# Performance work log

Measured on AMD Instinct MI355X. Metric: run time of the kernel, lower is better.

## Reference

```python
import jax, jax.numpy as jnp
import numpy as np
import math

B, T, IN_DIM, HID = 32, 1024, 512, 512
TAU_MEM = 20.0
THRESHOLD = 1.0
ALPHA = math.exp(-1.0 / TAU_MEM)


def setup_inputs() -> dict:
    key = jax.random.key(0)
    kx, kw, kb = jax.random.split(key, 3)
    bound = 1.0 / math.sqrt(IN_DIM)
    x = jax.random.normal(kx, (B, T, IN_DIM), dtype=jnp.float32)
    W = jax.random.uniform(kw, (HID, IN_DIM), minval=-bound, maxval=bound, dtype=jnp.float32)
    b = jax.random.uniform(kb, (HID,), minval=-bound, maxval=bound, dtype=jnp.float32)
    threshold_adapt = jnp.ones((HID,), dtype=jnp.float32) * THRESHOLD
    return {"x": x, "W": W, "b": b, "threshold_adapt": threshold_adapt}


def reference(x, W, b, threshold_adapt):
    # Precompute the batched GEMM for all timesteps: z[b,t,h]
    z = jnp.einsum('bti,hi->bth', x, W) + b
    thr = threshold_adapt[None, :]  # [1,H]

    def step(mem, z_t):
        # leaky integrate
        mem = ALPHA * mem + z_t              # [B,H]
        spike = (mem >= thr).astype(mem.dtype)
        mem = mem * (1.0 - spike)            # hard reset
        return mem, spike

    mem0 = jnp.zeros((x.shape[0], W.shape[0]), dtype=x.dtype)
    # scan over time axis: z transposed to [T,B,H]
    mem_final, spikes = jax.lax.scan(step, mem0, jnp.swapaxes(z, 0, 1))
    spikes = jnp.swapaxes(spikes, 0, 1)      # [B,T,H]
    return spikes, mem_final
```

## Files before the change

### kernel.cpp

```cpp
#include <hip/hip_runtime.h>
#include <cstdint>
#include <cstddef>

#define BATCH  32
#define TSTEPS 1024
#define INDIM  512
#define HIDDIM 512
#define MTOT   (BATCH * TSTEPS)

#define MB 128
#define NB 128
#define KC 32
#define KTILES (INDIM / KC)
#define NBLK   (HIDDIM / NB)

constexpr float ALPHA = 0.951229424500714f;

__device__ __forceinline__ int swzg(int g) { return g ^ (g >> 3); }

__global__ __launch_bounds__(256)
void snn_gemm(const float* __restrict__ x, const float* __restrict__ W,
              float* __restrict__ z)
{
    __shared__ float Asm[KC][MB];
    __shared__ float Bsm[KC][NB];

    const int tid = threadIdx.x;
    const int mb  = blockIdx.x / NBLK;
    const int nb  = blockIdx.x % NBLK;
    const int m0  = mb * MB;
    const int n0  = nb * NB;

    const int sr = tid >> 1;
    const int sc = (tid & 1) * 4;
    const int srg = sr >> 2;
    const int swr = (swzg(srg) << 2) | (sr & 3);

    const float4* Ag = reinterpret_cast<const float4*>(x + (size_t)(m0 + sr) * INDIM) + sc;
    const float4* Bg = reinterpret_cast<const float4*>(W + (size_t)(n0 + sr) * INDIM) + sc;

    const int cm = (tid >> 4) * 8;
    const int cn = (tid & 15) * 8;
    const int am0 = swzg(cm >> 2);
    const int am1 = swzg((cm >> 2) + 1);
    const int bn0 = swzg(cn >> 2);
    const int bn1 = swzg((cn >> 2) + 1);

    float acc[8][8];
#pragma unroll
    for (int i = 0; i < 8; ++i)
#pragma unroll
        for (int j = 0; j < 8; ++j) acc[i][j] = 0.0f;

    float4 sa[4], sb[4];
#pragma unroll
    for (int j = 0; j < 4; ++j) { sa[j] = Ag[j]; sb[j] = Bg[j]; }

    for (int kt = 0; kt < KTILES; ++kt) {
        __syncthreads();
#pragma unroll
        for (int j = 0; j < 4; ++j) {
            const int kq = (sc + j) * 4;
            Asm[kq + 0][swr] = sa[j].x;
            Asm[kq + 1][swr] = sa[j].y;
            Asm[kq + 2][swr] = sa[j].z;
            Asm[kq + 3][swr] = sa[j].w;
            Bsm[kq + 0][swr] = sb[j].x;
            Bsm[kq + 1][swr] = sb[j].y;
            Bsm[kq + 2][swr] = sb[j].z;
            Bsm[kq + 3][swr] = sb[j].w;
        }
        __syncthreads();

        if (kt + 1 < KTILES) {
            Ag += KC / 4;
            Bg += KC / 4;
#pragma unroll
            for (int j = 0; j < 4; ++j) { sa[j] = Ag[j]; sb[j] = Bg[j]; }
        }

#pragma unroll 8
        for (int kc = 0; kc < KC; ++kc) {
            const float4* Ar = reinterpret_cast<const float4*>(&Asm[kc][0]);
            const float4* Br = reinterpret_cast<const float4*>(&Bsm[kc][0]);
            float4 a0 = Ar[am0];
            float4 a1 = Ar[am1];
            float4 b0 = Br[bn0];
            float4 b1 = Br[bn1];
            const float av[8] = {a0.x, a0.y, a0.z, a0.w, a1.x, a1.y, a1.z, a1.w};
            const float bv[8] = {b0.x, b0.y, b0.z, b0.w, b1.x, b1.y, b1.z, b1.w};
#pragma unroll
            for (int i = 0; i < 8; ++i)
#pragma unroll
                for (int j = 0; j < 8; ++j)
                    acc[i][j] = fmaf(av[i], bv[j], acc[i][j]);
        }
    }

#pragma unroll
    for (int i = 0; i < 8; ++i) {
        float* zr = z + (size_t)(m0 + cm + i) * HIDDIM + n0 + cn;
        float4 v0 = {acc[i][0], acc[i][1], acc[i][2], acc[i][3]};
        float4 v1 = {acc[i][4], acc[i][5], acc[i][6], acc[i][7]};
        *reinterpret_cast<float4*>(zr)     = v0;
        *reinterpret_cast<float4*>(zr + 4) = v1;
    }
}

#define SCAND 8

__global__ __launch_bounds__(64)
void snn_scan(const float* zsrc, float* out,
              const float* __restrict__ bias, const float* __restrict__ thr)
{
    const int h = (blockIdx.x & 7) * 64 + threadIdx.x;
    const int b = blockIdx.x >> 3;

    const float bb = bias[h];
    const float tt = thr[h];
    float mem = 0.0f;

    const size_t base = ((size_t)b * TSTEPS) * HIDDIM + h;
    const float* zp = zsrc + base;
    float* sp = out + base;

    float pf[SCAND][8];

#pragma unroll
    for (int g = 0; g < SCAND; ++g)
#pragma unroll
        for (int j = 0; j < 8; ++j)
            pf[g][j] = zp[(size_t)(g * 8 + j) * HIDDIM];

#pragma unroll 8
    for (int t8 = 0; t8 < 120; ++t8) {
        const int slot = t8 & (SCAND - 1);
        float cur[8];
#pragma unroll
        for (int j = 0; j < 8; ++j) cur[j] = pf[slot][j];
#pragma unroll
        for (int j = 0; j < 8; ++j)
            pf[slot][j] = zp[(size_t)((t8 + SCAND) * 8 + j) * HIDDIM];
#pragma unroll
        for (int j = 0; j < 8; ++j) {
            float zv = cur[j] + bb;
            mem = fmaf(ALPHA, mem, zv);
            bool s = (mem >= tt);
            sp[(size_t)(t8 * 8 + j) * HIDDIM] = s ? 1.0f : 0.0f;
            mem = s ? 0.0f : mem;
        }
    }

#pragma unroll
    for (int t8 = 120; t8 < 128; ++t8) {
        const int slot = t8 & (SCAND - 1);
#pragma unroll
        for (int j = 0; j < 8; ++j) {
            float zv = pf[slot][j] + bb;
            mem = fmaf(ALPHA, mem, zv);
            bool s = (mem >= tt);
            sp[(size_t)(t8 * 8 + j) * HIDDIM] = s ? 1.0f : 0.0f;
            mem = s ? 0.0f : mem;
        }
    }

    out[(size_t)MTOT * HIDDIM + (size_t)b * HIDDIM + h] = mem;
}

extern "C" void kernel_launch(void* const* d_in, const int* in_sizes, int n_in,
                              void* d_out, int out_size, void* d_ws, size_t ws_size,
                              hipStream_t stream)
{
    const float* x    = (const float*)d_in[0];
    const float* W    = (const float*)d_in[1];
    const float* bias = (const float*)d_in[2];
    const float* thr  = (const float*)d_in[3];
    float* out = (float*)d_out;

    (void)in_sizes; (void)n_in; (void)out_size;

    const size_t z_bytes = (size_t)MTOT * HIDDIM * sizeof(float);
    const bool use_ws = (ws_size >= z_bytes);
    float* zbuf = use_ws ? (float*)d_ws : out;

    dim3 ggrid((MTOT / MB) * NBLK);
    hipLaunchKernelGGL(snn_gemm, ggrid, dim3(256), 0, stream, x, W, zbuf);

    dim3 sgrid(BATCH * (HIDDIM / 64));
    hipLaunchKernelGGL(snn_scan, sgrid, dim3(64), 0, stream, zbuf, out, bias, thr);
}
```

Measured before the change: 326.7 us.

## Warp-specialize scan kernel with producer wave staging z chunks into LDS

The recurrent scan kernel now uses 128-thread blocks. One wave issues vectorized float4 global loads of 32-timestep chunks of z into a double-buffered LDS tile, while the other wave runs the serial leaky-integrate recurrence reading from LDS. This replaces the per-thread scalar register prefetch ring. The goal is to hide global load latency behind the serial dependency chain and use wider loads. In exchange it adds a block barrier every chunk and LDS traffic, and only half the threads do the scan arithmetic.

```diff
diff --git a/kernel.cpp b/kernel.cpp
--- a/kernel.cpp
+++ b/kernel.cpp
@@ -13,6 +13,10 @@
 #define KC 32
 #define KTILES (INDIM / KC)
 #define NBLK   (HIDDIM / NB)
+
+#define SH 64
+#define ST 32
+#define SNC (TSTEPS / ST)
 
 constexpr float ALPHA = 0.951229424500714f;
 
@@ -41,10 +45,8 @@
 
     const int cm = (tid >> 4) * 8;
     const int cn = (tid & 15) * 8;
-    const int am0 = swzg(cm >> 2);
-    const int am1 = swzg((cm >> 2) + 1);
-    const int bn0 = swzg(cn >> 2);
-    const int bn1 = swzg((cn >> 2) + 1);
+    const int am0 = swzg(cm >> 2), am1 = swzg((cm >> 2) + 1);
+    const int bn0 = swzg(cn >> 2), bn1 = swzg((cn >> 2) + 1);
 
     float acc[8][8];
 #pragma unroll
@@ -107,64 +109,91 @@
     }
 }
 
-#define SCAND 8
-
-__global__ __launch_bounds__(64)
-void snn_scan(const float* zsrc, float* out,
+#define LWRITE(BUF, R)                                                        \
+    _Pragma("unroll")                                                         \
+    for (int j = 0; j < 8; ++j)                                               \
+        *reinterpret_cast<float4*>(&zl[BUF][j * 4 + tr][hc]) = R[j];
+
+#define GLOAD(R, C)                                                           \
+    _Pragma("unroll")                                                         \
+    for (int j = 0; j < 8; ++j)                                               \
+        R[j] = *reinterpret_cast<const float4*>(                              \
+            zbase + (size_t)((C) * ST + j * 4 + tr) * HIDDIM + hc);
+
+#define SCAN_CHUNK(BUF, C)                                                    \
+    {                                                                         \
+        float* orow = obase + (size_t)(C) * ST * HIDDIM + lane;               \
+        _Pragma("unroll 8")                                                   \
+        for (int r = 0; r < ST; ++r) {                                        \
+            float zv = zl[BUF][r][lane] + bb;                                 \
+            mem = fmaf(ALPHA, mem, zv);                                       \
+            bool s = (mem >= tt);                                             \
+            orow[(size_t)r * HIDDIM] = s ? 1.0f : 0.0f;                       \
+            mem = s ? 0.0f : mem;                                             \
+        }                                                                     \
+    }
+
+#define FENCE_BARRIER()                                                       \
+    asm volatile("s_waitcnt lgkmcnt(0)" ::: "memory");                        \
+    __builtin_amdgcn_sched_barrier(0);                                        \
+    __builtin_amdgcn_s_barrier();
+
+__global__ __launch_bounds__(128)
+void snn_scan(const float* __restrict__ zsrc, float* __restrict__ out,
               const float* __restrict__ bias, const float* __restrict__ thr)
 {
-    const int h = (blockIdx.x & 7) * 64 + threadIdx.x;
-    const int b = blockIdx.x >> 3;
-
-    const float bb = bias[h];
-    const float tt = thr[h];
+    __shared__ float zl[2][ST][SH];
+
+    const int tid  = threadIdx.x;
+    const int lane = tid & 63;
+    const int wave = tid >> 6;
+    const int b    = blockIdx.x >> 3;
+    const int h0   = (blockIdx.x & 7) * SH;
+
+    const float* zbase = zsrc + (size_t)b * TSTEPS * HIDDIM + h0;
+    float*       obase = out  + (size_t)b * TSTEPS * HIDDIM + h0;
+
+    const int tr = lane >> 4;
+    const int hc = (lane & 15) * 4;
+
+    const float bb = (wave == 0) ? bias[h0 + lane] : 0.0f;
+    const float tt = (wave == 0) ? thr[h0 + lane]  : 1.0e30f;
     float mem = 0.0f;
 
-    const size_t base = ((size_t)b * TSTEPS) * HIDDIM + h;
-    const float* zp = zsrc + base;
-    float* sp = out + base;
-
-    float pf[SCAND][8];
-
-#pragma unroll
-    for (int g = 0; g < SCAND; ++g)
-#pragma unroll
-        for (int j = 0; j < 8; ++j)
-            pf[g][j] = zp[(size_t)(g * 8 + j) * HIDDIM];
-
-#pragma unroll 8
-    for (int t8 = 0; t8 < 120; ++t8) {
-        const int slot = t8 & (SCAND - 1);
-        float cur[8];
-#pragma unroll
-        for (int j = 0; j < 8; ++j) cur[j] = pf[slot][j];
-#pragma unroll
-        for (int j = 0; j < 8; ++j)
-            pf[slot][j] = zp[(size_t)((t8 + SCAND) * 8 + j) * HIDDIM];
-#pragma unroll
-        for (int j = 0; j < 8; ++j) {
-            float zv = cur[j] + bb;
-            mem = fmaf(ALPHA, mem, zv);
-            bool s = (mem >= tt);
-            sp[(size_t)(t8 * 8 + j) * HIDDIM] = s ? 1.0f : 0.0f;
-            mem = s ? 0.0f : mem;
-        }
-    }
-
-#pragma unroll
-    for (int t8 = 120; t8 < 128; ++t8) {
-        const int slot = t8 & (SCAND - 1);
-#pragma unroll
-        for (int j = 0; j < 8; ++j) {
-            float zv = pf[slot][j] + bb;
-            mem = fmaf(ALPHA, mem, zv);
-            bool s = (mem >= tt);
-            sp[(size_t)(t8 * 8 + j) * HIDDIM] = s ? 1.0f : 0.0f;
-            mem = s ? 0.0f : mem;
-        }
-    }
-
-    out[(size_t)MTOT * HIDDIM + (size_t)b * HIDDIM + h] = mem;
+    float4 ra[8], rb[8];
+
+    if (wave == 1) {
+        GLOAD(ra, 0)
+        GLOAD(rb, 1)
+        __builtin_amdgcn_sched_barrier(0);
+        LWRITE(0, ra)
+    }
+    FENCE_BARRIER();
+
+    for (int cc = 0; cc < SNC / 2; ++cc) {
+        const int c = 2 * cc;
+
+        if (wave == 1) {
+            if (c + 2 < SNC) { GLOAD(ra, c + 2) }
+            __builtin_amdgcn_sched_barrier(0);
+            LWRITE(1, rb)
+        } else {
+            SCAN_CHUNK(0, c)
+        }
+        FENCE_BARRIER();
+
+        if (wave == 1) {
+            if (c + 3 < SNC) { GLOAD(rb, c + 3) }
+            __builtin_amdgcn_sched_barrier(0);
+            if (c + 2 < SNC) { LWRITE(0, ra) }
+        } else {
+            SCAN_CHUNK(1, c + 1)
+        }
+        FENCE_BARRIER();
+    }
+
+    if (wave == 0)
+        out[(size_t)MTOT * HIDDIM + (size_t)b * HIDDIM + h0 + lane] = mem;
 }
 
 extern "C" void kernel_launch(void* const* d_in, const int* in_sizes, int n_in,
@@ -180,12 +209,11 @@
     (void)in_sizes; (void)n_in; (void)out_size;
 
     const size_t z_bytes = (size_t)MTOT * HIDDIM * sizeof(float);
-    const bool use_ws = (ws_size >= z_bytes);
-    float* zbuf = use_ws ? (float*)d_ws : out;
+    float* zbuf = (ws_size >= z_bytes) ? (float*)d_ws : out;
 
     dim3 ggrid((MTOT / MB) * NBLK);
     hipLaunchKernelGGL(snn_gemm, ggrid, dim3(256), 0, stream, x, W, zbuf);
 
-    dim3 sgrid(BATCH * (HIDDIM / 64));
-    hipLaunchKernelGGL(snn_scan, sgrid, dim3(64), 0, stream, zbuf, out, bias, thr);
+    dim3 sgrid(BATCH * (HIDDIM / SH));
+    hipLaunchKernelGGL(snn_scan, sgrid, dim3(128), 0, stream, zbuf, out, bias, thr);
 }
```

After: 334.8 us. +2.5%, slower.

## Split scan over time segments chained through flag-based carry handoff

Applied to the files above, without the earlier changes.

Replaces the single-pass scan (256 blocks of 64 threads, each walking all 1024 timesteps) with 16 time segments per (batch, hidden-chunk). Each segment block preloads its 64 z values into registers, then spin-waits on an acquire flag until the previous segment publishes its membrane state, runs the short serial recurrence, releases its own carry and writes its spikes. The goal is to expose far more memory-level parallelism in the latency-bound scan, with only the cheap compute left on the serial chain. It adds a memset, workspace for carries and flags, and a possible deadlock if later segments occupy the device before earlier ones are scheduled.

```diff
diff --git a/kernel.cpp b/kernel.cpp
--- a/kernel.cpp
+++ b/kernel.cpp
@@ -14,6 +14,9 @@
 #define KTILES (INDIM / KC)
 #define NBLK   (HIDDIM / NB)
 
+#define NSEG 16
+#define SEGT (TSTEPS / NSEG)
+
 constexpr float ALPHA = 0.951229424500714f;
 
 __device__ __forceinline__ int swzg(int g) { return g ^ (g >> 3); }
@@ -41,10 +44,8 @@
 
     const int cm = (tid >> 4) * 8;
     const int cn = (tid & 15) * 8;
-    const int am0 = swzg(cm >> 2);
-    const int am1 = swzg((cm >> 2) + 1);
-    const int bn0 = swzg(cn >> 2);
-    const int bn1 = swzg((cn >> 2) + 1);
+    const int am0 = swzg(cm >> 2), am1 = swzg((cm >> 2) + 1);
+    const int bn0 = swzg(cn >> 2), bn1 = swzg((cn >> 2) + 1);
 
     float acc[8][8];
 #pragma unroll
@@ -107,11 +108,67 @@
     }
 }
 
-#define SCAND 8
+__global__ __launch_bounds__(64, 4)
+void snn_scan_chain(const float* __restrict__ z, float* __restrict__ out,
+                    const float* __restrict__ bias, const float* __restrict__ thr,
+                    float* __restrict__ mem_buf, unsigned int* __restrict__ flags)
+{
+    const int lane = threadIdx.x;
+    const int bid  = blockIdx.x;
+    const int seg  = bid >> 8;
+    const int bh   = bid & 255;
+    const int b    = bh >> 3;
+    const int h0   = (bh & 7) * 64;
+    const int h    = h0 + lane;
+    const int cidx = bh * NSEG + seg;
+
+    const float* zp = z + ((size_t)b * TSTEPS + seg * SEGT) * HIDDIM + h;
+    float zr[SEGT];
+#pragma unroll
+    for (int j = 0; j < SEGT; ++j) zr[j] = zp[(size_t)j * HIDDIM];
+
+    const float bb = bias[h];
+    const float tt = thr[h];
+
+    float mem = 0.0f;
+    if (seg > 0) {
+        const unsigned int* fp = &flags[cidx - 1];
+        while (__hip_atomic_load(fp, __ATOMIC_ACQUIRE, __HIP_MEMORY_SCOPE_AGENT) == 0u)
+            __builtin_amdgcn_s_sleep(8);
+        mem = mem_buf[(size_t)(cidx - 1) * 64 + lane];
+    }
+
+    unsigned int w0 = 0u, w1 = 0u;
+#pragma unroll
+    for (int j = 0; j < SEGT; ++j) {
+        float zv = zr[j] + bb;
+        mem = fmaf(ALPHA, mem, zv);
+        bool s = (mem >= tt);
+        if (j < 32) { w0 |= s ? (1u << j) : 0u; }
+        else        { w1 |= s ? (1u << (j - 32)) : 0u; }
+        mem = s ? 0.0f : mem;
+    }
+
+    if (seg + 1 < NSEG) {
+        mem_buf[(size_t)cidx * 64 + lane] = mem;
+        if (lane == 0)
+            __hip_atomic_store(&flags[cidx], 1u, __ATOMIC_RELEASE,
+                               __HIP_MEMORY_SCOPE_AGENT);
+    } else {
+        out[(size_t)MTOT * HIDDIM + (size_t)b * HIDDIM + h] = mem;
+    }
+
+    float* ob = out + ((size_t)b * TSTEPS + seg * SEGT) * HIDDIM + h;
+#pragma unroll 8
+    for (int j = 0; j < SEGT; ++j) {
+        unsigned int bit = (j < 32) ? ((w0 >> j) & 1u) : ((w1 >> (j - 32)) & 1u);
+        ob[(size_t)j * HIDDIM] = bit ? 1.0f : 0.0f;
+    }
+}
 
 __global__ __launch_bounds__(64)
-void snn_scan(const float* zsrc, float* out,
-              const float* __restrict__ bias, const float* __restrict__ thr)
+void snn_scan_fb(const float* zsrc, float* out,
+                 const float* __restrict__ bias, const float* __restrict__ thr)
 {
     const int h = (blockIdx.x & 7) * 64 + threadIdx.x;
     const int b = blockIdx.x >> 3;
@@ -124,46 +181,19 @@
     const float* zp = zsrc + base;
     float* sp = out + base;
 
-    float pf[SCAND][8];
-
-#pragma unroll
-    for (int g = 0; g < SCAND; ++g)
-#pragma unroll
-        for (int j = 0; j < 8; ++j)
-            pf[g][j] = zp[(size_t)(g * 8 + j) * HIDDIM];
-
-#pragma unroll 8
-    for (int t8 = 0; t8 < 120; ++t8) {
-        const int slot = t8 & (SCAND - 1);
-        float cur[8];
-#pragma unroll
-        for (int j = 0; j < 8; ++j) cur[j] = pf[slot][j];
-#pragma unroll
-        for (int j = 0; j < 8; ++j)
-            pf[slot][j] = zp[(size_t)((t8 + SCAND) * 8 + j) * HIDDIM];
+    for (int t = 0; t < TSTEPS; t += 8) {
+        float zl[8];
+#pragma unroll
+        for (int j = 0; j < 8; ++j) zl[j] = zp[(size_t)(t + j) * HIDDIM];
 #pragma unroll
         for (int j = 0; j < 8; ++j) {
-            float zv = cur[j] + bb;
+            float zv = zl[j] + bb;
             mem = fmaf(ALPHA, mem, zv);
             bool s = (mem >= tt);
-            sp[(size_t)(t8 * 8 + j) * HIDDIM] = s ? 1.0f : 0.0f;
+            sp[(size_t)(t + j) * HIDDIM] = s ? 1.0f : 0.0f;
             mem = s ? 0.0f : mem;
         }
     }
-
-#pragma unroll
-    for (int t8 = 120; t8 < 128; ++t8) {
-        const int slot = t8 & (SCAND - 1);
-#pragma unroll
-        for (int j = 0; j < 8; ++j) {
-            float zv = pf[slot][j] + bb;
-            mem = fmaf(ALPHA, mem, zv);
-            bool s = (mem >= tt);
-            sp[(size_t)(t8 * 8 + j) * HIDDIM] = s ? 1.0f : 0.0f;
-            mem = s ? 0.0f : mem;
-        }
-    }
-
     out[(size_t)MTOT * HIDDIM + (size_t)b * HIDDIM + h] = mem;
 }
 
@@ -179,13 +209,26 @@
 
     (void)in_sizes; (void)n_in; (void)out_size;
 
-    const size_t z_bytes = (size_t)MTOT * HIDDIM * sizeof(float);
-    const bool use_ws = (ws_size >= z_bytes);
-    float* zbuf = use_ws ? (float*)d_ws : out;
+    const size_t z_bytes    = (size_t)MTOT * HIDDIM * sizeof(float);
+    const size_t mem_bytes  = (size_t)256 * NSEG * 64 * sizeof(float);
+    const size_t flag_bytes = (size_t)256 * NSEG * sizeof(unsigned int);
+    const size_t need = z_bytes + mem_bytes + flag_bytes;
 
     dim3 ggrid((MTOT / MB) * NBLK);
-    hipLaunchKernelGGL(snn_gemm, ggrid, dim3(256), 0, stream, x, W, zbuf);
-
-    dim3 sgrid(BATCH * (HIDDIM / 64));
-    hipLaunchKernelGGL(snn_scan, sgrid, dim3(64), 0, stream, zbuf, out, bias, thr);
-}
+
+    if (ws_size >= need) {
+        float* zbuf   = (float*)d_ws;
+        float* membuf = (float*)((char*)d_ws + z_bytes);
+        unsigned int* flags = (unsigned int*)((char*)d_ws + z_bytes + mem_bytes);
+
+        hipMemsetAsync(flags, 0, flag_bytes, stream);
+
+        hipLaunchKernelGGL(snn_gemm, ggrid, dim3(256), 0, stream, x, W, zbuf);
+        hipLaunchKernelGGL(snn_scan_chain, dim3(NSEG * 256), dim3(64), 0, stream,
+                           zbuf, out, bias, thr, membuf, flags);
+    } else {
+        hipLaunchKernelGGL(snn_gemm, ggrid, dim3(256), 0, stream, x, W, out);
+        hipLaunchKernelGGL(snn_scan_fb, dim3(BATCH * 8), dim3(64), 0, stream,
+                           out, out, bias, thr);
+    }
+}
```

After: 1.118 ms. 3.42x slower.
